# Kernel tuning notes

Hardware: AMD Instinct MI355X
Metric: run time of the kernel (lower is better)

Reference implementation:

```python
import jax, jax.numpy as jnp
import numpy as np

B, S, C = 256, 169, 512      # batch, input seq_len (hardcoded 169 in source), n_attn
H, TT, HS = 256, 256, 16     # n_head, ctx_len, head_size (all forced by hardcoded shapes)
OUT = 64                     # output Linear(16, 64)


def setup_inputs() -> dict:
    key = jax.random.key(0)
    ks = jax.random.split(key, 13)
    s_in = 1.0 / np.sqrt(C)
    s_hs = 1.0 / np.sqrt(HS)
    return {
        "x": jax.random.normal(ks[0], (B, S, C), dtype=jnp.float32),
        "time_w": jax.random.normal(ks[1], (H, TT), dtype=jnp.float32) * 0.1,
        "time_alpha": jax.random.normal(ks[2], (H, 1, TT), dtype=jnp.float32) * 0.1 + 1.0,
        "time_beta": jax.random.normal(ks[3], (H, TT, 1), dtype=jnp.float32) * 0.1 + 1.0,
        "time_gamma": jax.random.normal(ks[4], (TT, 1), dtype=jnp.float32) * 0.1 + 1.0,
        "key_w": jax.random.normal(ks[5], (HS, C), dtype=jnp.float32) * s_in,
        "key_b": jax.random.normal(ks[6], (HS,), dtype=jnp.float32) * s_in,
        "value_w": jax.random.normal(ks[7], (HS, C), dtype=jnp.float32) * s_in,
        "value_b": jax.random.normal(ks[8], (HS,), dtype=jnp.float32) * s_in,
        "recep_w": jax.random.normal(ks[9], (HS, C), dtype=jnp.float32) * s_in,
        "recep_b": jax.random.normal(ks[10], (HS,), dtype=jnp.float32) * s_in,
        "out_w": jax.random.normal(ks[11], (OUT, HS), dtype=jnp.float32) * s_hs,
        "out_b": jax.random.normal(ks[12], (OUT,), dtype=jnp.float32) * s_hs,
    }


def reference(x, time_w, time_alpha, time_beta, time_gamma,
              key_w, key_b, value_w, value_b, recep_w, recep_b,
              out_w, out_b):
    # --- build the time-decay matrix via the pad/tile shift trick ---
    w = jnp.pad(time_w, ((0, 0), (0, TT)))            # (H, 2TT)
    w = jnp.tile(w, (1, TT))                          # (H, 2TT*TT)
    w = w[:, :-TT].reshape(H, TT, 2 * TT - 1)
    w = w[:, :, TT - 1:]                              # (H, TT, TT)
    w = w * time_alpha * time_beta                    # (H, TT, TT)

    # --- channel-half time shift: first C/2 channels shifted back by 1 step ---
    half = C // 2
    shifted = jnp.pad(x[:, :, :half], ((0, 0), (1, 0), (0, 0)))[:, :-1]
    x = jnp.concatenate([shifted, x[:, :, half:]], axis=-1)

    # --- projections (torch Linear: y = x @ W.T + b) ---
    k = x @ key_w.T + key_b                           # (B, S, HS)
    v = x @ value_w.T + value_b
    r = x @ recep_w.T + recep_b

    pad_len = TT - S                                  # 256 - 169 = 87
    r = jnp.pad(r, ((0, 0), (0, pad_len), (0, 0)))    # (B, TT, HS)

    k = jnp.exp(jnp.clip(k, -60.0, 30.0))
    sum_k = jnp.cumsum(k, axis=1)                     # (B, S, HS)
    sum_k = jnp.pad(sum_k, ((0, 0), (0, pad_len), (0, 0)))  # (B, TT, HS)

    kv = k * v                                        # (B, S, HS)
    kv = jnp.pad(kv, ((0, 0), (0, pad_len), (0, 0)))  # (B, TT, HS)

    # einsum('htu,bhc->btc') == contract u first, then (t,h) matmul against kv's seq axis
    w2 = w.sum(axis=-1)                               # (H, TT): sum_u w[h,t,u]
    wkv = jnp.einsum('ht,bhc->btc', w2, kv)           # (B, TT, HS)

    # original divides by zero-padded sum_k in the padded tail; guard with 1 there
    denom = jnp.where(sum_k == 0, jnp.ones_like(sum_k), sum_k)
    rwkv = jax.nn.sigmoid(r) * wkv / denom            # (B, TT, HS)

    rwkv = rwkv @ out_w.T + out_b                     # (B, TT, 64)
    rwkv = rwkv * time_gamma[:TT]                     # (TT,1) broadcast
    return rwkv
```

## Files before the change

kernel.cpp:

```cpp
#include <hip/hip_runtime.h>

typedef unsigned short u16;
typedef unsigned int u32;
typedef __attribute__((ext_vector_type(8))) __bf16 bf16x8;
typedef __attribute__((ext_vector_type(4))) float f32x4;

#define S_LEN 169
#define SP 192

#define W2T_WS 0
#define WPK_WS 98304
#define KE_WS  147456
#define KV_WS  3031040
#define SG_WS  5914624

#define WT_OFF  0
#define XT0_OFF 49152
#define XT1_OFF 61440
#define G_LDS   73728

#define SKE  0
#define SKV  11264
#define SG2  22528
#define SKVT 33792
#define SRB  39936
#define SSS  60416
#define SOW  61440
#define S_LDS 66560

#define LGKM_BAR() asm volatile("s_waitcnt lgkmcnt(0)\n\ts_barrier" ::: "memory")

__global__ __launch_bounds__(1024) void w2_kernel(
    const float* __restrict__ time_w,
    const float* __restrict__ time_alpha,
    const float* __restrict__ time_beta,
    const float* __restrict__ key_w,
    const float* __restrict__ value_w,
    const float* __restrict__ recep_w,
    char* __restrict__ ws)
{
    __bf16* w2t = (__bf16*)(ws + W2T_WS);
    const int blk = blockIdx.x;
    if (blk >= 192) {
        int p = blk - 192;
        int u = threadIdx.x;
        if (u < 768) {
            int j  = 12 * p + (u >> 6);
            int co = (u & 63) << 3;
            const float* src;
            if (j < 16)      src = key_w   + j * 512 + co;
            else if (j < 32) src = value_w + (j - 16) * 512 + co;
            else             src = recep_w + (j - 32) * 512 + co;
            float4 f0 = *(const float4*)src;
            float4 f1 = *(const float4*)(src + 4);
            bf16x8 pk;
            pk[0]=(__bf16)f0.x; pk[1]=(__bf16)f0.y; pk[2]=(__bf16)f0.z; pk[3]=(__bf16)f0.w;
            pk[4]=(__bf16)f1.x; pk[5]=(__bf16)f1.y; pk[6]=(__bf16)f1.z; pk[7]=(__bf16)f1.w;
            u32 off = (((u32)j << 10) + ((u32)co << 1)) ^ (((u32)(j & 7)) << 4);
            *(bf16x8*)(ws + WPK_WS + off) = pk;
        }
        return;
    }
    __shared__ float tw[256];
    __shared__ float al[256];
    __shared__ float part[4][256];
    const int s = blk;
    const int t = threadIdx.x & 255;
    const int p = threadIdx.x >> 8;
    if (s >= S_LEN) {
        if (p == 0) w2t[t * SP + s] = (__bf16)0.f;
        return;
    }
    if (p == 0) { tw[t] = time_w[s * 256 + t]; al[t] = time_alpha[s * 256 + t]; }
    __syncthreads();
    const int u0 = p << 6;
    const int u1 = (u0 + 64 < t + 1) ? (u0 + 64) : (t + 1);
    float acc = 0.f;
    for (int u = u0; u < u1; ++u)
        acc = fmaf(tw[255 + u - t], al[u], acc);
    part[p][t] = acc;
    __syncthreads();
    if (p == 0)
        w2t[t * SP + s] = (__bf16)(time_beta[s * 256 + t] *
                                   (part[0][t] + part[1][t] + part[2][t] + part[3][t]));
}

__global__ __launch_bounds__(256) void gemm_kernel(
    const float* __restrict__ x,
    const float* __restrict__ key_b,
    const float* __restrict__ value_b,
    const float* __restrict__ recep_b,
    const char* __restrict__ wsr,
    char* __restrict__ ws)
{
    __shared__ __align__(16) char smem[G_LDS];
    const int tid  = threadIdx.x;
    const int lane = tid & 63;
    const int wid  = tid >> 6;
    const int q    = lane >> 4;
    const int hs   = lane & 15;
    const int b    = blockIdx.x >> 1;
    const int half = blockIdx.x & 1;
    const int t0   = half * 88;
    const int nrows = half ? 81 : 88;
    const float* xb = x + (size_t)b * (S_LEN * 512);

    #pragma unroll
    for (int it = 0; it < 12; ++it) {
        int i = tid + (it << 8);
        uint4 cp = *(const uint4*)(wsr + WPK_WS + i * 16);
        *(uint4*)(smem + WT_OFF + i * 16) = cp;
    }

    const float kb = key_b[hs];
    const float vb = value_b[hs];
    const float rb = recep_b[hs];

    f32x4 acc0[3], acc1[3];
    #pragma unroll
    for (int n = 0; n < 3; ++n) { acc0[n] = (f32x4){0.f,0.f,0.f,0.f}; acc1[n] = (f32x4){0.f,0.f,0.f,0.f}; }
    const bool has_m1 = (wid < 2);

    float4 pfA[3][2]; int pvA[3];
    float4 pfB[3][2]; int pvB[3];

    auto ldchunk = [&](int chunk, float4 (&pf)[3][2], int (&pv)[3]) {
        const bool shifted = chunk < 4;
        #pragma unroll
        for (int it = 0; it < 3; ++it) {
            int i = tid + (it << 8);
            int r = i >> 3;
            bool valid = shifted ? (r < nrows && (t0 + r) >= 1) : (r < nrows);
            pv[it] = valid ? 1 : 0;
            if (valid) {
                int tsrc = t0 + r - (shifted ? 1 : 0);
                const float* src = xb + (size_t)tsrc * 512 + (chunk << 6) + ((i & 7) << 3);
                pf[it][0] = *(const float4*)src;
                pf[it][1] = *(const float4*)(src + 4);
            }
        }
    };

    auto cvtwrite = [&](u32 base, float4 (&pf)[3][2], int (&pv)[3]) {
        #pragma unroll
        for (int it = 0; it < 3; ++it) {
            int i = tid + (it << 8);
            int r = i >> 3, co = (i & 7) << 3;
            bf16x8 p = {(__bf16)0.f,(__bf16)0.f,(__bf16)0.f,(__bf16)0.f,
                        (__bf16)0.f,(__bf16)0.f,(__bf16)0.f,(__bf16)0.f};
            if (pv[it]) {
                p[0]=(__bf16)pf[it][0].x; p[1]=(__bf16)pf[it][0].y;
                p[2]=(__bf16)pf[it][0].z; p[3]=(__bf16)pf[it][0].w;
                p[4]=(__bf16)pf[it][1].x; p[5]=(__bf16)pf[it][1].y;
                p[6]=(__bf16)pf[it][1].z; p[7]=(__bf16)pf[it][1].w;
            }
            u32 off = (((u32)r << 7) + ((u32)co << 1)) ^ (((u32)(r & 7)) << 4);
            *(bf16x8*)(smem + base + off) = p;
        }
    };

    auto mfma_chunk = [&](int chunk, u32 xbase) {
        #pragma unroll
        for (int ks = 0; ks < 2; ++ks) {
            int kc = ks << 5;
            bf16x8 bfr[3];
            #pragma unroll
            for (int nt = 0; nt < 3; ++nt) {
                int j = nt * 16 + hs;
                u32 col = (u32)((chunk << 6) + kc + (q << 3));
                u32 off = (((u32)j << 10) + (col << 1)) ^ (((u32)(j & 7)) << 4);
                bfr[nt] = *(const bf16x8*)(smem + WT_OFF + off);
            }
            {
                int row = wid * 16 + hs;
                u32 off = (((u32)row << 7) + ((u32)(kc + (q << 3)) << 1)) ^ (((u32)(row & 7)) << 4);
                bf16x8 afr = *(const bf16x8*)(smem + xbase + off);
                acc0[0] = __builtin_amdgcn_mfma_f32_16x16x32_bf16(afr, bfr[0], acc0[0], 0,0,0);
                acc0[1] = __builtin_amdgcn_mfma_f32_16x16x32_bf16(afr, bfr[1], acc0[1], 0,0,0);
                acc0[2] = __builtin_amdgcn_mfma_f32_16x16x32_bf16(afr, bfr[2], acc0[2], 0,0,0);
            }
            if (has_m1) {
                int row = (wid + 4) * 16 + hs;
                u32 off = (((u32)row << 7) + ((u32)(kc + (q << 3)) << 1)) ^ (((u32)(row & 7)) << 4);
                bf16x8 afr = *(const bf16x8*)(smem + xbase + off);
                acc1[0] = __builtin_amdgcn_mfma_f32_16x16x32_bf16(afr, bfr[0], acc1[0], 0,0,0);
                acc1[1] = __builtin_amdgcn_mfma_f32_16x16x32_bf16(afr, bfr[1], acc1[1], 0,0,0);
                acc1[2] = __builtin_amdgcn_mfma_f32_16x16x32_bf16(afr, bfr[2], acc1[2], 0,0,0);
            }
        }
    };

    ldchunk(0, pfA, pvA);
    cvtwrite(XT0_OFF, pfA, pvA);
    ldchunk(1, pfA, pvA);
    ldchunk(2, pfB, pvB);
    LGKM_BAR();

    #pragma unroll
    for (int chunk = 0; chunk < 8; ++chunk) {
        const u32 cur = (chunk & 1) ? XT1_OFF : XT0_OFF;
        const u32 nxt = (chunk & 1) ? XT0_OFF : XT1_OFF;
        mfma_chunk(chunk, cur);
        if (chunk < 7) {
            if (chunk & 1) cvtwrite(nxt, pfB, pvB);
            else           cvtwrite(nxt, pfA, pvA);
        }
        LGKM_BAR();
        if (chunk < 5) {
            if (chunk & 1) ldchunk(chunk + 3, pfB, pvB);
            else           ldchunk(chunk + 3, pfA, pvA);
        }
    }

    float* keg = (float*)(ws + KE_WS);
    float* kvg = (float*)(ws + KV_WS);
    float* sgg = (float*)(ws + SG_WS);
    #pragma unroll
    for (int m = 0; m < 2; ++m) {
        if (m == 1 && !has_m1) break;
        const f32x4* A = (m == 0) ? acc0 : acc1;
        int tl = (wid + m * 4) * 16 + (q << 2);
        #pragma unroll
        for (int rg = 0; rg < 4; ++rg) {
            int t_local = tl + rg;
            if (t_local < nrows) {
                int t = t0 + t_local;
                float kk = fminf(fmaxf(A[0][rg] + kb, -60.f), 30.f);
                float ke = __expf(kk);
                size_t o = ((size_t)b * 176 + t) * 16 + hs;
                keg[o] = ke;
                kvg[o] = ke * (A[1][rg] + vb);
                sgg[o] = 1.f / (1.f + __expf(-(A[2][rg] + rb)));
            }
        }
    }
}

__global__ __launch_bounds__(256) void scan_kernel(
    const char* __restrict__ wsr,
    const float* __restrict__ out_w, const float* __restrict__ out_b,
    const float* __restrict__ gamma,
    float* __restrict__ out)
{
    __shared__ __align__(16) char smem[S_LDS];
    const int tid  = threadIdx.x;
    const int lane = tid & 63;
    const int wid  = tid >> 6;
    const int q    = lane >> 4;
    const int hs   = lane & 15;
    const int b    = blockIdx.x;
    const __bf16* w2t = (const __bf16*)(wsr + W2T_WS);
    const float4* keb = (const float4*)(wsr + KE_WS + (size_t)b * 11264);
    const float4* kvb = (const float4*)(wsr + KV_WS + (size_t)b * 11264);
    const float4* sgb = (const float4*)(wsr + SG_WS + (size_t)b * 11264);

    #pragma unroll
    for (int it = 0; it < 3; ++it) {
        int i = tid + (it << 8);
        if (i < 676) {
            ((float4*)(smem + SKE))[i] = keb[i];
            ((float4*)(smem + SKV))[i] = kvb[i];
            ((float4*)(smem + SG2))[i] = sgb[i];
        }
    }
    for (int i = tid; i < 2560; i += 256) {
        int o = i / 40, c = i - o * 40;
        ((__bf16*)(smem + SOW))[i] = (c < 16) ? (__bf16)out_w[o * 16 + c] : (__bf16)0.f;
    }
    for (int i = tid; i < 4096; i += 256) {
        int row = i >> 4, c = 16 + (i & 15);
        ((__bf16*)(smem + SRB))[row * 40 + c] = (__bf16)0.f;
    }
    for (int i = tid; i < 368; i += 256) {
        int h2 = i & 15; int t = S_LEN + (i >> 4);
        u32 off = ((u32)(h2 * 384 + t * 2)) ^ (((u32)(h2 & 7)) << 4);
        *(__bf16*)(smem + SKVT + off) = (__bf16)0.f;
    }
    __syncthreads();

    float* KE = (float*)(smem + SKE);
    float* KV = (float*)(smem + SKV);
    float* GG = (float*)(smem + SG2);
    float* SEG = (float*)(smem + SSS);
    const int h  = tid & 15;
    const int sg = tid >> 4;
    const int ts = sg * 11;
    const int te = (ts + 11 < S_LEN) ? ts + 11 : S_LEN;
    {
        float ssum = 0.f;
        for (int t = ts; t < te; ++t) ssum += KE[t * 16 + h];
        SEG[sg * 16 + h] = ssum;
    }
    __syncthreads();
    {
        float run = 0.f;
        for (int s2 = 0; s2 < sg; ++s2) run += SEG[s2 * 16 + h];
        for (int t = ts; t < te; ++t) {
            run += KE[t * 16 + h];
            u32 off = ((u32)(h * 384 + t * 2)) ^ (((u32)(h & 7)) << 4);
            *(__bf16*)(smem + SKVT + off) = (__bf16)KV[t * 16 + h];
            GG[t * 16 + h] = GG[t * 16 + h] / run;
        }
    }
    __syncthreads();

    f32x4 wa[4];
    #pragma unroll
    for (int mi = 0; mi < 4; ++mi) wa[mi] = (f32x4){0.f,0.f,0.f,0.f};
    #pragma unroll
    for (int s0 = 0; s0 < SP; s0 += 32) {
        int scol = s0 + (q << 3);
        u32 boff = ((u32)(hs * 384 + scol * 2)) ^ (((u32)(hs & 7)) << 4);
        bf16x8 bfr = *(const bf16x8*)(smem + SKVT + boff);
        #pragma unroll
        for (int mi = 0; mi < 4; ++mi) {
            int row = (wid + (mi << 2)) * 16 + hs;
            bf16x8 afr = *(const bf16x8*)(w2t + row * SP + scol);
            wa[mi] = __builtin_amdgcn_mfma_f32_16x16x32_bf16(afr, bfr, wa[mi], 0,0,0);
        }
    }
    #pragma unroll
    for (int mi = 0; mi < 4; ++mi) {
        int tb = (wid + (mi << 2)) * 16 + (q << 2);
        #pragma unroll
        for (int rg = 0; rg < 4; ++rg) {
            int t = tb + rg;
            float fac = (t < S_LEN) ? GG[t * 16 + hs] : 0.5f;
            ((__bf16*)(smem + SRB))[t * 40 + hs] = (__bf16)(wa[mi][rg] * fac);
        }
    }
    __syncthreads();

    float obv[4];
    #pragma unroll
    for (int nt = 0; nt < 4; ++nt) obv[nt] = out_b[nt * 16 + hs];
    #pragma unroll
    for (int mi = 0; mi < 4; ++mi) {
        int mt = wid + (mi << 2);
        int arow = mt * 16 + hs;
        bf16x8 afr = *(const bf16x8*)(smem + SRB + (u32)(arow * 80 + (q << 4)));
        float gm[4];
        #pragma unroll
        for (int rg = 0; rg < 4; ++rg) gm[rg] = gamma[mt * 16 + (q << 2) + rg];
        #pragma unroll
        for (int nt = 0; nt < 4; ++nt) {
            int orow = nt * 16 + hs;
            bf16x8 bfr = *(const bf16x8*)(smem + SOW + (u32)(orow * 80 + (q << 4)));
            f32x4 zc = (f32x4){0.f,0.f,0.f,0.f};
            f32x4 d = __builtin_amdgcn_mfma_f32_16x16x32_bf16(afr, bfr, zc, 0,0,0);
            #pragma unroll
            for (int rg = 0; rg < 4; ++rg) {
                int t = mt * 16 + (q << 2) + rg;
                out[(size_t)b * 16384 + (size_t)t * 64 + nt * 16 + hs] = (d[rg] + obv[nt]) * gm[rg];
            }
        }
    }
}

extern "C" void kernel_launch(void* const* d_in, const int* in_sizes, int n_in,
                              void* d_out, int out_size, void* d_ws, size_t ws_size,
                              hipStream_t stream) {
    const float* x          = (const float*)d_in[0];
    const float* time_w     = (const float*)d_in[1];
    const float* time_alpha = (const float*)d_in[2];
    const float* time_beta  = (const float*)d_in[3];
    const float* time_gamma = (const float*)d_in[4];
    const float* key_w      = (const float*)d_in[5];
    const float* key_b      = (const float*)d_in[6];
    const float* value_w    = (const float*)d_in[7];
    const float* value_b    = (const float*)d_in[8];
    const float* recep_w    = (const float*)d_in[9];
    const float* recep_b    = (const float*)d_in[10];
    const float* out_w      = (const float*)d_in[11];
    const float* out_b      = (const float*)d_in[12];
    char* ws = (char*)d_ws;

    w2_kernel<<<196, 1024, 0, stream>>>(time_w, time_alpha, time_beta,
                                        key_w, value_w, recep_w, ws);
    gemm_kernel<<<512, 256, 0, stream>>>(x, key_b, value_b, recep_b, ws, ws);
    scan_kernel<<<256, 256, 0, stream>>>(ws, out_w, out_b, time_gamma, (float*)d_out);
}
```

Baseline: 41.61 us.

## Fuse decay-matrix build and projection GEMM into one kernel with register-resident weights

The separate w2 and gemm kernels are merged into a single launch. The first 192 blocks build the decay matrix, and the remaining blocks compute the projections for 32-row time slabs per batch, one wave per projection. Weights are loaded straight from global memory and converted to bf16 fragments held in registers, which removes the pre-packed weight staging pass and one kernel launch. The x tile is staged once with the channel-half shift handled by row offsets, and outputs go through LDS for coalesced writes. The trade-off is more blocks, redundant weight loads per block, and slower single-thread decay rows that now run inside the same launch.

```diff
diff --git a/kernel.cpp b/kernel.cpp
--- a/kernel.cpp
+++ b/kernel.cpp
@@ -3,21 +3,16 @@
 typedef unsigned short u16;
 typedef unsigned int u32;
 typedef __attribute__((ext_vector_type(8))) __bf16 bf16x8;
+typedef __attribute__((ext_vector_type(4))) __bf16 bf16x4;
 typedef __attribute__((ext_vector_type(4))) float f32x4;
 
 #define S_LEN 169
 #define SP 192
 
 #define W2T_WS 0
-#define WPK_WS 98304
-#define KE_WS  147456
-#define KV_WS  3031040
-#define SG_WS  5914624
-
-#define WT_OFF  0
-#define XT0_OFF 49152
-#define XT1_OFF 61440
-#define G_LDS   73728
+#define KE_WS  98304
+#define KV_WS  (98304 + 2883584)
+#define SG_WS  (98304 + 2 * 2883584)
 
 #define SKE  0
 #define SKV  11264
@@ -28,209 +23,134 @@
 #define SOW  61440
 #define S_LDS 66560
 
-#define LGKM_BAR() asm volatile("s_waitcnt lgkmcnt(0)\n\ts_barrier" ::: "memory")
-
-__global__ __launch_bounds__(1024) void w2_kernel(
+__global__ __launch_bounds__(192, 3) void k1_kernel(
+    const float* __restrict__ x,
     const float* __restrict__ time_w,
     const float* __restrict__ time_alpha,
     const float* __restrict__ time_beta,
-    const float* __restrict__ key_w,
-    const float* __restrict__ value_w,
-    const float* __restrict__ recep_w,
+    const float* __restrict__ key_w,  const float* __restrict__ key_b,
+    const float* __restrict__ value_w,const float* __restrict__ value_b,
+    const float* __restrict__ recep_w,const float* __restrict__ recep_b,
     char* __restrict__ ws)
 {
+    __shared__ __align__(16) char smem[33792];
+    const int tid = threadIdx.x;
     __bf16* w2t = (__bf16*)(ws + W2T_WS);
-    const int blk = blockIdx.x;
-    if (blk >= 192) {
-        int p = blk - 192;
-        int u = threadIdx.x;
-        if (u < 768) {
-            int j  = 12 * p + (u >> 6);
-            int co = (u & 63) << 3;
-            const float* src;
-            if (j < 16)      src = key_w   + j * 512 + co;
-            else if (j < 32) src = value_w + (j - 16) * 512 + co;
-            else             src = recep_w + (j - 32) * 512 + co;
-            float4 f0 = *(const float4*)src;
-            float4 f1 = *(const float4*)(src + 4);
-            bf16x8 pk;
-            pk[0]=(__bf16)f0.x; pk[1]=(__bf16)f0.y; pk[2]=(__bf16)f0.z; pk[3]=(__bf16)f0.w;
-            pk[4]=(__bf16)f1.x; pk[5]=(__bf16)f1.y; pk[6]=(__bf16)f1.z; pk[7]=(__bf16)f1.w;
-            u32 off = (((u32)j << 10) + ((u32)co << 1)) ^ (((u32)(j & 7)) << 4);
-            *(bf16x8*)(ws + WPK_WS + off) = pk;
+    int blk = blockIdx.x;
+
+    if (blk < 192) {
+        const int s = blk;
+        if (s >= S_LEN) {
+            for (int t = tid; t < 256; t += 192) w2t[t * SP + s] = (__bf16)0.f;
+            return;
+        }
+        float* tw = (float*)smem;
+        float* al = (float*)(smem + 1024);
+        for (int i = tid; i < 256; i += 192) {
+            tw[i] = time_w[s * 256 + i];
+            al[i] = time_alpha[s * 256 + i];
+        }
+        __syncthreads();
+        for (int t = tid; t < 256; t += 192) {
+            float acc = 0.f;
+            for (int u = 0; u <= t; ++u)
+                acc = fmaf(tw[255 + u - t], al[u], acc);
+            w2t[t * SP + s] = (__bf16)(time_beta[s * 256 + t] * acc);
         }
         return;
     }
-    __shared__ float tw[256];
-    __shared__ float al[256];
-    __shared__ float part[4][256];
-    const int s = blk;
-    const int t = threadIdx.x & 255;
-    const int p = threadIdx.x >> 8;
-    if (s >= S_LEN) {
-        if (p == 0) w2t[t * SP + s] = (__bf16)0.f;
-        return;
-    }
-    if (p == 0) { tw[t] = time_w[s * 256 + t]; al[t] = time_alpha[s * 256 + t]; }
-    __syncthreads();
-    const int u0 = p << 6;
-    const int u1 = (u0 + 64 < t + 1) ? (u0 + 64) : (t + 1);
-    float acc = 0.f;
-    for (int u = u0; u < u1; ++u)
-        acc = fmaf(tw[255 + u - t], al[u], acc);
-    part[p][t] = acc;
-    __syncthreads();
-    if (p == 0)
-        w2t[t * SP + s] = (__bf16)(time_beta[s * 256 + t] *
-                                   (part[0][t] + part[1][t] + part[2][t] + part[3][t]));
-}
-
-__global__ __launch_bounds__(256) void gemm_kernel(
-    const float* __restrict__ x,
-    const float* __restrict__ key_b,
-    const float* __restrict__ value_b,
-    const float* __restrict__ recep_b,
-    const char* __restrict__ wsr,
-    char* __restrict__ ws)
-{
-    __shared__ __align__(16) char smem[G_LDS];
-    const int tid  = threadIdx.x;
+
+    blk -= 192;
+    const int b    = blk / 6;
+    const int slab = blk - b * 6;
+    const int t0   = slab * 32;
     const int lane = tid & 63;
-    const int wid  = tid >> 6;
+    const int wv   = tid >> 6;
     const int q    = lane >> 4;
     const int hs   = lane & 15;
-    const int b    = blockIdx.x >> 1;
-    const int half = blockIdx.x & 1;
-    const int t0   = half * 88;
-    const int nrows = half ? 81 : 88;
     const float* xb = x + (size_t)b * (S_LEN * 512);
 
-    #pragma unroll
-    for (int it = 0; it < 12; ++it) {
-        int i = tid + (it << 8);
-        uint4 cp = *(const uint4*)(wsr + WPK_WS + i * 16);
-        *(uint4*)(smem + WT_OFF + i * 16) = cp;
-    }
-
-    const float kb = key_b[hs];
-    const float vb = value_b[hs];
-    const float rb = recep_b[hs];
-
-    f32x4 acc0[3], acc1[3];
-    #pragma unroll
-    for (int n = 0; n < 3; ++n) { acc0[n] = (f32x4){0.f,0.f,0.f,0.f}; acc1[n] = (f32x4){0.f,0.f,0.f,0.f}; }
-    const bool has_m1 = (wid < 2);
-
-    float4 pfA[3][2]; int pvA[3];
-    float4 pfB[3][2]; int pvB[3];
-
-    auto ldchunk = [&](int chunk, float4 (&pf)[3][2], int (&pv)[3]) {
-        const bool shifted = chunk < 4;
-        #pragma unroll
-        for (int it = 0; it < 3; ++it) {
-            int i = tid + (it << 8);
-            int r = i >> 3;
-            bool valid = shifted ? (r < nrows && (t0 + r) >= 1) : (r < nrows);
-            pv[it] = valid ? 1 : 0;
-            if (valid) {
-                int tsrc = t0 + r - (shifted ? 1 : 0);
-                const float* src = xb + (size_t)tsrc * 512 + (chunk << 6) + ((i & 7) << 3);
-                pf[it][0] = *(const float4*)src;
-                pf[it][1] = *(const float4*)(src + 4);
-            }
-        }
-    };
-
-    auto cvtwrite = [&](u32 base, float4 (&pf)[3][2], int (&pv)[3]) {
-        #pragma unroll
-        for (int it = 0; it < 3; ++it) {
-            int i = tid + (it << 8);
-            int r = i >> 3, co = (i & 7) << 3;
-            bf16x8 p = {(__bf16)0.f,(__bf16)0.f,(__bf16)0.f,(__bf16)0.f,
-                        (__bf16)0.f,(__bf16)0.f,(__bf16)0.f,(__bf16)0.f};
-            if (pv[it]) {
-                p[0]=(__bf16)pf[it][0].x; p[1]=(__bf16)pf[it][0].y;
-                p[2]=(__bf16)pf[it][0].z; p[3]=(__bf16)pf[it][0].w;
-                p[4]=(__bf16)pf[it][1].x; p[5]=(__bf16)pf[it][1].y;
-                p[6]=(__bf16)pf[it][1].z; p[7]=(__bf16)pf[it][1].w;
-            }
-            u32 off = (((u32)r << 7) + ((u32)co << 1)) ^ (((u32)(r & 7)) << 4);
-            *(bf16x8*)(smem + base + off) = p;
-        }
-    };
-
-    auto mfma_chunk = [&](int chunk, u32 xbase) {
-        #pragma unroll
-        for (int ks = 0; ks < 2; ++ks) {
-            int kc = ks << 5;
-            bf16x8 bfr[3];
-            #pragma unroll
-            for (int nt = 0; nt < 3; ++nt) {
-                int j = nt * 16 + hs;
-                u32 col = (u32)((chunk << 6) + kc + (q << 3));
-                u32 off = (((u32)j << 10) + (col << 1)) ^ (((u32)(j & 7)) << 4);
-                bfr[nt] = *(const bf16x8*)(smem + WT_OFF + off);
-            }
-            {
-                int row = wid * 16 + hs;
-                u32 off = (((u32)row << 7) + ((u32)(kc + (q << 3)) << 1)) ^ (((u32)(row & 7)) << 4);
-                bf16x8 afr = *(const bf16x8*)(smem + xbase + off);
-                acc0[0] = __builtin_amdgcn_mfma_f32_16x16x32_bf16(afr, bfr[0], acc0[0], 0,0,0);
-                acc0[1] = __builtin_amdgcn_mfma_f32_16x16x32_bf16(afr, bfr[1], acc0[1], 0,0,0);
-                acc0[2] = __builtin_amdgcn_mfma_f32_16x16x32_bf16(afr, bfr[2], acc0[2], 0,0,0);
-            }
-            if (has_m1) {
-                int row = (wid + 4) * 16 + hs;
-                u32 off = (((u32)row << 7) + ((u32)(kc + (q << 3)) << 1)) ^ (((u32)(row & 7)) << 4);
-                bf16x8 afr = *(const bf16x8*)(smem + xbase + off);
-                acc1[0] = __builtin_amdgcn_mfma_f32_16x16x32_bf16(afr, bfr[0], acc1[0], 0,0,0);
-                acc1[1] = __builtin_amdgcn_mfma_f32_16x16x32_bf16(afr, bfr[1], acc1[1], 0,0,0);
-                acc1[2] = __builtin_amdgcn_mfma_f32_16x16x32_bf16(afr, bfr[2], acc1[2], 0,0,0);
-            }
-        }
-    };
-
-    ldchunk(0, pfA, pvA);
-    cvtwrite(XT0_OFF, pfA, pvA);
-    ldchunk(1, pfA, pvA);
-    ldchunk(2, pfB, pvB);
-    LGKM_BAR();
-
-    #pragma unroll
-    for (int chunk = 0; chunk < 8; ++chunk) {
-        const u32 cur = (chunk & 1) ? XT1_OFF : XT0_OFF;
-        const u32 nxt = (chunk & 1) ? XT0_OFF : XT1_OFF;
-        mfma_chunk(chunk, cur);
-        if (chunk < 7) {
-            if (chunk & 1) cvtwrite(nxt, pfB, pvB);
-            else           cvtwrite(nxt, pfA, pvA);
-        }
-        LGKM_BAR();
-        if (chunk < 5) {
-            if (chunk & 1) ldchunk(chunk + 3, pfB, pvB);
-            else           ldchunk(chunk + 3, pfA, pvA);
-        }
-    }
+    #pragma unroll 4
+    for (int u = 0; u < 22; ++u) {
+        int i   = tid + u * 192;
+        int row = i >> 7;
+        int cu  = i & 127;
+        int g   = t0 - 1 + row;
+        float4 f = {0.f, 0.f, 0.f, 0.f};
+        if (g >= 0 && g < S_LEN) f = *(const float4*)(xb + (size_t)g * 512 + cu * 4);
+        bf16x4 p;
+        p[0] = (__bf16)f.x; p[1] = (__bf16)f.y; p[2] = (__bf16)f.z; p[3] = (__bf16)f.w;
+        u32 off = ((u32)row << 10) + ((((u32)cu) << 3) ^ (((u32)(row & 7)) << 4));
+        *(bf16x4*)(smem + off) = p;
+    }
+
+    const float* wmat = (wv == 0) ? key_w : (wv == 1) ? value_w : recep_w;
+    const float* bvec = (wv == 0) ? key_b : (wv == 1) ? value_b : recep_b;
+    bf16x8 bfrag[16];
+    #pragma unroll
+    for (int ksb = 0; ksb < 16; ksb += 4) {
+        float4 w0[4], w1[4];
+        #pragma unroll
+        for (int j = 0; j < 4; ++j) {
+            const float* src = wmat + hs * 512 + (ksb + j) * 32 + q * 8;
+            w0[j] = *(const float4*)src;
+            w1[j] = *(const float4*)(src + 4);
+        }
+        #pragma unroll
+        for (int j = 0; j < 4; ++j) {
+            bf16x8 p;
+            p[0]=(__bf16)w0[j].x; p[1]=(__bf16)w0[j].y; p[2]=(__bf16)w0[j].z; p[3]=(__bf16)w0[j].w;
+            p[4]=(__bf16)w1[j].x; p[5]=(__bf16)w1[j].y; p[6]=(__bf16)w1[j].z; p[7]=(__bf16)w1[j].w;
+            bfrag[ksb + j] = p;
+        }
+    }
+    __syncthreads();
+
+    f32x4 acc0 = (f32x4){0.f,0.f,0.f,0.f};
+    f32x4 acc1 = (f32x4){0.f,0.f,0.f,0.f};
+    #pragma unroll
+    for (int ks = 0; ks < 16; ++ks) {
+        u32 colb = ((u32)(ks * 32 + q * 8)) << 1;
+        int r0 = hs + ((ks < 8) ? 0 : 1);
+        u32 off0 = ((u32)r0 << 10) + (colb ^ (((u32)(r0 & 7)) << 4));
+        bf16x8 a0 = *(const bf16x8*)(smem + off0);
+        acc0 = __builtin_amdgcn_mfma_f32_16x16x32_bf16(a0, bfrag[ks], acc0, 0, 0, 0);
+        int r1 = r0 + 16;
+        u32 off1 = ((u32)r1 << 10) + (colb ^ (((u32)(r1 & 7)) << 4));
+        bf16x8 a1 = *(const bf16x8*)(smem + off1);
+        acc1 = __builtin_amdgcn_mfma_f32_16x16x32_bf16(a1, bfrag[ks], acc1, 0, 0, 0);
+    }
+    __syncthreads();
+
+    float* raw = (float*)smem;
+    const float bias = bvec[hs];
+    #pragma unroll
+    for (int m = 0; m < 2; ++m) {
+        f32x4 A = m ? acc1 : acc0;
+        #pragma unroll
+        for (int rg = 0; rg < 4; ++rg) {
+            int lt = m * 16 + q * 4 + rg;
+            raw[wv * 512 + lt * 16 + hs] = A[rg] + bias;
+        }
+    }
+    __syncthreads();
 
     float* keg = (float*)(ws + KE_WS);
     float* kvg = (float*)(ws + KV_WS);
     float* sgg = (float*)(ws + SG_WS);
     #pragma unroll
-    for (int m = 0; m < 2; ++m) {
-        if (m == 1 && !has_m1) break;
-        const f32x4* A = (m == 0) ? acc0 : acc1;
-        int tl = (wid + m * 4) * 16 + (q << 2);
-        #pragma unroll
-        for (int rg = 0; rg < 4; ++rg) {
-            int t_local = tl + rg;
-            if (t_local < nrows) {
-                int t = t0 + t_local;
-                float kk = fminf(fmaxf(A[0][rg] + kb, -60.f), 30.f);
+    for (int u = 0; u < 3; ++u) {
+        int i = tid + u * 192;
+        if (i < 512) {
+            int lt = i >> 4, h = i & 15;
+            int t = t0 + lt;
+            if (t < S_LEN) {
+                float kk = fminf(fmaxf(raw[i], -60.f), 30.f);
                 float ke = __expf(kk);
-                size_t o = ((size_t)b * 176 + t) * 16 + hs;
+                size_t o = ((size_t)b * 176 + t) * 16 + h;
                 keg[o] = ke;
-                kvg[o] = ke * (A[1][rg] + vb);
-                sgg[o] = 1.f / (1.f + __expf(-(A[2][rg] + rb)));
+                kvg[o] = ke * raw[512 + i];
+                sgg[o] = 1.f / (1.f + __expf(-raw[1024 + i]));
             }
         }
     }
@@ -375,8 +295,8 @@
     const float* out_b      = (const float*)d_in[12];
     char* ws = (char*)d_ws;
 
-    w2_kernel<<<196, 1024, 0, stream>>>(time_w, time_alpha, time_beta,
-                                        key_w, value_w, recep_w, ws);
-    gemm_kernel<<<512, 256, 0, stream>>>(x, key_b, value_b, recep_b, ws, ws);
+    k1_kernel<<<1728, 192, 0, stream>>>(x, time_w, time_alpha, time_beta,
+                                        key_w, key_b, value_w, value_b,
+                                        recep_w, recep_b, ws);
     scan_kernel<<<256, 256, 0, stream>>>(ws, out_w, out_b, time_gamma, (float*)d_out);
 }
```

After: 55.86 us. +34.3%, slower.
